# Kernel tuning notes

Measured on AMD Instinct MI355X. Metric: run time of the kernel, lower is better.

The kernel has to match this reference:

```python
import jax, jax.numpy as jnp
import numpy as np

K = 16          # neighbors per query (args.k)
EPS_NORM = 1e-5  # LayerNorm / BatchNorm eps (torch default)


def _knn_edges(xyz, B, n):
    # batch-aware kNN: equal-sized batches, edges never cross batch boundary
    x = xyz.reshape(B, n, 3)
    d2 = jnp.sum((x[:, :, None, :] - x[:, None, :, :]) ** 2, -1)   # [B,n,n]
    _, idx = jax.lax.top_k(-d2, K)                                 # [B,n,K] local neighbor ids
    col = (idx + (jnp.arange(B) * n)[:, None, None]).reshape(-1)   # source (neighbor) [E]
    row = jnp.repeat(jnp.arange(B * n), K)                         # target (query)    [E]
    return row, col


def _forward(support_xyz, batch_index, features, lang_features, mask_flattened,
             W1, b1, ln_g, ln_b, W2, b2,
             Wl1, bl1, bn_g, bn_b, Wl2, bl2,
             Wr1, br1, Wr2, br2, row, col):
    N = support_xyz.shape[0]
    B, L, Fl = lang_features.shape
    # feat_encoder: Linear -> LayerNorm -> ReLU -> Linear
    h = features @ W1 + b1
    mu = h.mean(-1, keepdims=True)
    var = ((h - mu) ** 2).mean(-1, keepdims=True)
    h = (h - mu) / jnp.sqrt(var + EPS_NORM) * ln_g + ln_b
    feats = jax.nn.relu(h) @ W2 + b2                               # [N,F]
    # lang_encoder: Linear -> BatchNorm1d (batch statistics) -> ReLU -> Linear
    hl = lang_features.reshape(B * L, Fl) @ Wl1 + bl1
    mul = hl.mean(0)
    varl = ((hl - mul) ** 2).mean(0)
    hl = (hl - mul) / jnp.sqrt(varl + EPS_NORM) * bn_g + bn_b
    lang = (jax.nn.relu(hl) @ Wl2 + bl2).reshape(B, L, -1)         # [B,L,F]
    lang_flat = lang[batch_index]                                  # [N,L,F]
    # per-point / per-token attention logits
    atten = jnp.einsum('nf,nlf->nl', feats, lang_flat)             # [N,L]
    # segment softmax over incoming kNN edges (CenterOp max / add)
    attenmax = jax.ops.segment_max(atten[col], row, num_segments=N, indices_are_sorted=True)
    a = jnp.exp(atten[col] - attenmax[row])                        # [E,L]
    attensum = jax.ops.segment_sum(a, row, num_segments=N, indices_are_sorted=True)
    # CenterConv message
    att = a / attensum[row] * mask_flattened[row]                  # [E,L]
    att = att / (att.sum(-1, keepdims=True) + 1e-7)
    ctx = jnp.einsum('el,elf->ef', att, lang_flat[col])            # [E,F] attended lang feat
    xi, xj = support_xyz[row], support_xyz[col]
    d = xi - xj
    nrm = jnp.sqrt(jnp.sum(d * d, -1, keepdims=True) + 1e-12)
    ew = jnp.concatenate([xi, xj, d, nrm], -1)                     # [E,10]
    ew = jax.nn.relu(ew @ Wr1 + br1) @ Wr2 + br2                   # [E,F] rel_encoder
    msg = feats[col] * ctx * ew                                    # [E,F]
    rel = jax.ops.segment_sum(msg, row, num_segments=N, indices_are_sorted=True)
    return feats + rel


def setup_inputs() -> dict:
    key = jax.random.key(0)
    ks = jax.random.split(key, 12)
    B, n, L = 4, 1024, 16
    N = B * n
    Fv, Fl, F = 256, 768, 128
    def w(k, shp, fan):
        return jax.random.normal(k, shp, jnp.float32) / np.sqrt(fan).astype(np.float32)
    mask = (jax.random.uniform(ks[3], (N, L)) < 0.8).astype(jnp.float32).at[:, 0].set(1.0)
    return {
        'support_xyz': jax.random.normal(ks[0], (N, 3), jnp.float32),
        'batch_index': jnp.repeat(jnp.arange(B), n),
        'features': jax.random.normal(ks[1], (N, Fv), jnp.float32),
        'lang_features': jax.random.normal(ks[2], (B, L, Fl), jnp.float32),
        'mask_flattened': mask,
        'W1': w(ks[4], (Fv, F), Fv), 'b1': jnp.zeros(F, jnp.float32),
        'ln_g': jnp.ones(F, jnp.float32), 'ln_b': jnp.zeros(F, jnp.float32),
        'W2': w(ks[5], (F, F), F), 'b2': jnp.zeros(F, jnp.float32),
        'Wl1': w(ks[6], (Fl, F), Fl), 'bl1': jnp.zeros(F, jnp.float32),
        'bn_g': jnp.ones(F, jnp.float32), 'bn_b': jnp.zeros(F, jnp.float32),
        'Wl2': w(ks[7], (F, F), F), 'bl2': jnp.zeros(F, jnp.float32),
        'Wr1': w(ks[8], (10, 64), 10), 'br1': jnp.zeros(64, jnp.float32),
        'Wr2': w(ks[9], (64, F), 64), 'br2': jnp.zeros(F, jnp.float32),
    }


def reference(support_xyz, batch_index, features, lang_features, mask_flattened,
              W1, b1, ln_g, ln_b, W2, b2,
              Wl1, bl1, bn_g, bn_b, Wl2, bl2,
              Wr1, br1, Wr2, br2):
    B = lang_features.shape[0]
    n = support_xyz.shape[0] // B
    row, col = _knn_edges(support_xyz, B, n)
    return _forward(support_xyz, batch_index, features, lang_features, mask_flattened,
                    W1, b1, ln_g, ln_b, W2, b2,
                    Wl1, bl1, bn_g, bn_b, Wl2, bl2,
                    Wr1, br1, Wr2, br2, row, col)
```

## Files before the change

### kernel.cpp

```cpp
#include <hip/hip_runtime.h>

typedef unsigned long long u64;
typedef short short8 __attribute__((ext_vector_type(8)));
typedef float f32x4 __attribute__((ext_vector_type(4)));

#define N_PTS   4096
#define B_SZ    4
#define N_PER_B 1024
#define L_TOK   16
#define FV      256
#define FL      768
#define FDIM    128
#define KNN     16
#define RH      64

__device__ __forceinline__ short f2bf(float f) {
    unsigned int x = __float_as_uint(f);
    unsigned int r = (x + 0x7fffu + ((x >> 16) & 1u)) >> 16;
    return (short)r;
}

__global__ __launch_bounds__(256) void k1_kernel(const float* __restrict__ xyz,
                                                 const float* __restrict__ features,
                                                 const float* __restrict__ lf,
                                                 const float* __restrict__ W1,
                                                 const float* __restrict__ b1,
                                                 const float* __restrict__ ln_g,
                                                 const float* __restrict__ ln_b,
                                                 const float* __restrict__ W2,
                                                 const float* __restrict__ b2,
                                                 const float* __restrict__ Wl1,
                                                 const float* __restrict__ bl1,
                                                 int* __restrict__ knn,
                                                 float* __restrict__ feats,
                                                 float* __restrict__ hl) {
    __shared__ float smem[4 * 256 + 4 * 128 + 16];
    int b = blockIdx.x, t = threadIdx.x;

    if (b < 1024) {
        int lane = t & 63;
        int q = b * 4 + (t >> 6);
        int base = (q >> 10) << 10;
        float qx = xyz[q * 3 + 0];
        float qy = xyz[q * 3 + 1];
        float qz = xyz[q * 3 + 2];
        u64 keys[16];
#pragma unroll
        for (int m = 0; m < 16; m++) {
            int j = base + lane + (m << 6);
            float dx = qx - xyz[j * 3 + 0];
            float dy = qy - xyz[j * 3 + 1];
            float dz = qz - xyz[j * 3 + 2];
            float d2 = __fadd_rn(__fadd_rn(__fmul_rn(dx, dx), __fmul_rn(dy, dy)),
                                 __fmul_rn(dz, dz));
            keys[m] = (((u64)__float_as_uint(d2)) << 32) | (unsigned int)j;
        }
        for (int r = 0; r < KNN; r++) {
            u64 lmin = keys[0];
#pragma unroll
            for (int m = 1; m < 16; m++) lmin = (keys[m] < lmin) ? keys[m] : lmin;
            u64 g = lmin;
#pragma unroll
            for (int off = 32; off > 0; off >>= 1) {
                u64 o = __shfl_xor(g, off, 64);
                g = (o < g) ? o : g;
            }
#pragma unroll
            for (int m = 0; m < 16; m++)
                if (keys[m] == g) keys[m] = ~0ULL;
            if (lane == 0) knn[q * KNN + r] = (int)(g & 0xffffffffu);
        }
    } else if (b < 2048) {
        int i0 = (b - 1024) * 4;
        float* fin  = smem;
        float* rbuf = smem + 1024;
        float* red  = smem + 1536;
        for (int p = t; p < 4 * FV; p += 256) {
            int pp = p >> 8, k = p & 255;
            fin[pp * FV + k] = features[(i0 + pp) * FV + k];
        }
        __syncthreads();
        int c = t & 127, h = t >> 7;
        int p0 = 2 * h, p1 = 2 * h + 1;
        float bv = b1[c];
        float acc0 = bv, acc1 = bv;
        for (int k = 0; k < FV; k++) {
            float w = W1[k * FDIM + c];
            acc0 += fin[p0 * FV + k] * w;
            acc1 += fin[p1 * FV + k] * w;
        }
        float s0 = acc0, q0 = acc0 * acc0, s1 = acc1, q1 = acc1 * acc1;
#pragma unroll
        for (int off = 32; off > 0; off >>= 1) {
            s0 += __shfl_xor(s0, off, 64);
            q0 += __shfl_xor(q0, off, 64);
            s1 += __shfl_xor(s1, off, 64);
            q1 += __shfl_xor(q1, off, 64);
        }
        int wid = t >> 6;
        if ((t & 63) == 0) {
            red[wid * 4 + 0] = s0; red[wid * 4 + 1] = q0;
            red[wid * 4 + 2] = s1; red[wid * 4 + 3] = q1;
        }
        __syncthreads();
        float S0 = red[(2 * h) * 4 + 0] + red[(2 * h + 1) * 4 + 0];
        float Q0 = red[(2 * h) * 4 + 1] + red[(2 * h + 1) * 4 + 1];
        float S1 = red[(2 * h) * 4 + 2] + red[(2 * h + 1) * 4 + 2];
        float Q1 = red[(2 * h) * 4 + 3] + red[(2 * h + 1) * 4 + 3];
        float g = ln_g[c], bb = ln_b[c];
        float mu0 = S0 * (1.f / 128.f), var0 = Q0 * (1.f / 128.f) - mu0 * mu0;
        float mu1 = S1 * (1.f / 128.f), var1 = Q1 * (1.f / 128.f) - mu1 * mu1;
        float r0 = fmaxf((acc0 - mu0) * rsqrtf(var0 + 1e-5f) * g + bb, 0.f);
        float r1 = fmaxf((acc1 - mu1) * rsqrtf(var1 + 1e-5f) * g + bb, 0.f);
        rbuf[p0 * FDIM + c] = r0;
        rbuf[p1 * FDIM + c] = r1;
        __syncthreads();
        float b2v = b2[c];
        float f0 = b2v, f1 = b2v;
        for (int k = 0; k < FDIM; k++) {
            float w = W2[k * FDIM + c];
            f0 += rbuf[p0 * FDIM + k] * w;
            f1 += rbuf[p1 * FDIM + k] * w;
        }
        feats[(i0 + p0) * FDIM + c] = f0;
        feats[(i0 + p1) * FDIM + c] = f1;
    } else {
        int r = b - 2048;
        float* lrow = smem;
        float* part = smem + 768;
        for (int k = t; k < FL; k += 256) lrow[k] = lf[r * FL + k];
        __syncthreads();
        int c = t & 127, kh = t >> 7;
        float acc = (kh == 0) ? bl1[c] : 0.f;
        int k0 = kh * 384;
        for (int k = k0; k < k0 + 384; k++) acc += lrow[k] * Wl1[k * FDIM + c];
        part[kh * FDIM + c] = acc;
        __syncthreads();
        if (kh == 0) hl[r * FDIM + c] = part[c] + part[FDIM + c];
    }
}

__global__ __launch_bounds__(128) void lang2_kernel(const float* __restrict__ hl,
                                                    const float* __restrict__ bn_g,
                                                    const float* __restrict__ bn_b,
                                                    const float* __restrict__ Wl2,
                                                    const float* __restrict__ bl2,
                                                    float* __restrict__ lang) {
    __shared__ float rl4[4][FDIM];
    int t = threadIdx.x;
    int r0 = blockIdx.x * 4;
    float s = 0.f, s2 = 0.f;
    for (int r = 0; r < 64; r++) {
        float v = hl[r * FDIM + t];
        s += v; s2 += v * v;
    }
    float mu = s * (1.f / 64.f);
    float var = s2 * (1.f / 64.f) - mu * mu;
    float rs = rsqrtf(var + 1e-5f);
    float g = bn_g[t], bb = bn_b[t];
#pragma unroll
    for (int p = 0; p < 4; p++)
        rl4[p][t] = fmaxf((hl[(r0 + p) * FDIM + t] - mu) * rs * g + bb, 0.f);
    __syncthreads();
    float bv = bl2[t];
    float a0 = bv, a1 = bv, a2 = bv, a3 = bv;
    for (int k = 0; k < FDIM; k++) {
        float w = Wl2[k * FDIM + t];
        a0 += rl4[0][k] * w;
        a1 += rl4[1][k] * w;
        a2 += rl4[2][k] * w;
        a3 += rl4[3][k] * w;
    }
    lang[(r0 + 0) * FDIM + t] = a0;
    lang[(r0 + 1) * FDIM + t] = a1;
    lang[(r0 + 2) * FDIM + t] = a2;
    lang[(r0 + 3) * FDIM + t] = a3;
}

__global__ __launch_bounds__(256) void atten_kernel(const float* __restrict__ feats,
                                                    const float* __restrict__ lang,
                                                    float* __restrict__ atten) {
    __shared__ float fb[2][FDIM];
    __shared__ float pb[256];
    int t = threadIdx.x;
    int half = t >> 7, tt = t & 127;
    int i = blockIdx.x * 2 + half;
    fb[half][tt] = feats[i * FDIM + tt];
    __syncthreads();
    int l = tt >> 3, sj = tt & 7;
    int bi = i >> 10;
    const float* lrow = lang + (bi * L_TOK + l) * FDIM;
    float p = 0.f;
#pragma unroll
    for (int m = 0; m < 16; m++) {
        int k = sj + (m << 3);
        p += fb[half][k] * lrow[k];
    }
    pb[t] = p;
    __syncthreads();
    if (tt < L_TOK) {
        float a = 0.f;
#pragma unroll
        for (int u = 0; u < 8; u++) a += pb[half * 128 + tt * 8 + u];
        atten[i * L_TOK + tt] = a;
    }
}

__global__ __launch_bounds__(256) void edge_kernel(const float* __restrict__ xyz,
                                                   const float* __restrict__ mask,
                                                   const float* __restrict__ Wr1,
                                                   const float* __restrict__ br1,
                                                   const float* __restrict__ Wr2,
                                                   const float* __restrict__ br2,
                                                   const int* __restrict__ knn,
                                                   const float* __restrict__ lang,
                                                   const float* __restrict__ feats,
                                                   const float* __restrict__ atten,
                                                   float* __restrict__ out) {
    int lane = threadIdx.x & 63;
    int wid  = threadIdx.x >> 6;
    int i    = blockIdx.x * 4 + wid;
    int bi   = i >> 10;
    int quad = lane >> 4;
    int e16  = lane & 15;

    int idxe = knn[i * KNN + e16];

    float sat[8];
    if (quad < 2) {
        const float4* ap = (const float4*)(atten + idxe * L_TOK + quad * 8);
        float4 a0 = ap[0], a1 = ap[1];
        sat[0] = a0.x; sat[1] = a0.y; sat[2] = a0.z; sat[3] = a0.w;
        sat[4] = a1.x; sat[5] = a1.y; sat[6] = a1.z; sat[7] = a1.w;
    } else {
#pragma unroll
        for (int j = 0; j < 8; j++) sat[j] = 0.f;
    }

    float mx[8];
#pragma unroll
    for (int j = 0; j < 8; j++) mx[j] = sat[j];
#pragma unroll
    for (int off = 1; off < 16; off <<= 1) {
#pragma unroll
        for (int j = 0; j < 8; j++) mx[j] = fmaxf(mx[j], __shfl_xor(mx[j], off, 16));
    }
    float ex[8], sm[8];
#pragma unroll
    for (int j = 0; j < 8; j++) { ex[j] = __expf(sat[j] - mx[j]); sm[j] = ex[j]; }
#pragma unroll
    for (int off = 1; off < 16; off <<= 1) {
#pragma unroll
        for (int j = 0; j < 8; j++) sm[j] += __shfl_xor(sm[j], off, 16);
    }
    float st[8];
    if (quad < 2) {
        const float4* mp = (const float4*)(mask + i * L_TOK + quad * 8);
        float4 m0 = mp[0], m1 = mp[1];
        float mv[8] = {m0.x, m0.y, m0.z, m0.w, m1.x, m1.y, m1.z, m1.w};
#pragma unroll
        for (int j = 0; j < 8; j++) st[j] = ex[j] * (mv[j] / sm[j]);
    } else {
#pragma unroll
        for (int j = 0; j < 8; j++) st[j] = 0.f;
    }
    float s = st[0] + st[1] + st[2] + st[3] + st[4] + st[5] + st[6] + st[7];
    s += __shfl_xor(s, 16, 64);
    s += __shfl_xor(s, 32, 64);
    float inv2 = 1.f / (s + 1e-7f);
    short8 sattA;
#pragma unroll
    for (int j = 0; j < 8; j++) sattA[j] = f2bf(st[j] * inv2);

    float xi0 = xyz[i * 3 + 0], xi1 = xyz[i * 3 + 1], xi2 = xyz[i * 3 + 2];
    float xj0 = xyz[idxe * 3 + 0], xj1 = xyz[idxe * 3 + 1], xj2 = xyz[idxe * 3 + 2];
    float d0 = xi0 - xj0, d1 = xi1 - xj1, d2v = xi2 - xj2;
    float nr = sqrtf(d0 * d0 + d1 * d1 + d2v * d2v + 1e-12f);
    float ein[10] = {xi0, xi1, xi2, xj0, xj1, xj2, d0, d1, d2v, nr};
    short8 hidA[2];
#pragma unroll
    for (int sstep = 0; sstep < 2; sstep++) {
        int k0 = sstep * 32 + quad * 8;
        float h[8];
        const float4* bp = (const float4*)(br1 + k0);
        float4 b0 = bp[0], b1v = bp[1];
        h[0] = b0.x; h[1] = b0.y; h[2] = b0.z; h[3] = b0.w;
        h[4] = b1v.x; h[5] = b1v.y; h[6] = b1v.z; h[7] = b1v.w;
#pragma unroll
        for (int m = 0; m < 10; m++) {
            const float4* wp = (const float4*)(Wr1 + m * RH + k0);
            float4 w0 = wp[0], w1 = wp[1];
            float em = ein[m];
            h[0] += em * w0.x; h[1] += em * w0.y; h[2] += em * w0.z; h[3] += em * w0.w;
            h[4] += em * w1.x; h[5] += em * w1.y; h[6] += em * w1.z; h[7] += em * w1.w;
        }
#pragma unroll
        for (int j = 0; j < 8; j++) hidA[sstep][j] = f2bf(fmaxf(h[j], 0.f));
    }

    int idxr[4];
#pragma unroll
    for (int r = 0; r < 4; r++) idxr[r] = knn[i * KNN + quad * 4 + r];

#pragma unroll 2
    for (int tile = 0; tile < 8; tile++) {
        int cc = tile * 16 + e16;
        f32x4 accew = {0.f, 0.f, 0.f, 0.f};
#pragma unroll
        for (int sstep = 0; sstep < 2; sstep++) {
            short8 w2B;
#pragma unroll
            for (int j = 0; j < 8; j++)
                w2B[j] = f2bf(Wr2[(sstep * 32 + quad * 8 + j) * FDIM + cc]);
            accew = __builtin_amdgcn_mfma_f32_16x16x32_bf16(hidA[sstep], w2B, accew, 0, 0, 0);
        }
        short8 lsB;
        if (quad < 2) {
#pragma unroll
            for (int j = 0; j < 8; j++)
                lsB[j] = f2bf(lang[bi * L_TOK * FDIM + (quad * 8 + j) * FDIM + cc]);
        } else {
#pragma unroll
            for (int j = 0; j < 8; j++) lsB[j] = 0;
        }
        f32x4 accctx = {0.f, 0.f, 0.f, 0.f};
        accctx = __builtin_amdgcn_mfma_f32_16x16x32_bf16(sattA, lsB, accctx, 0, 0, 0);

        float br2c = br2[cc];
        float msum = 0.f;
#pragma unroll
        for (int r = 0; r < 4; r++) {
            float fj = feats[idxr[r] * FDIM + cc];
            msum += fj * accctx[r] * (accew[r] + br2c);
        }
        msum += __shfl_xor(msum, 16, 64);
        msum += __shfl_xor(msum, 32, 64);
        if (lane < 16)
            out[i * FDIM + cc] = feats[i * FDIM + cc] + msum;
    }
}

extern "C" void kernel_launch(void* const* d_in, const int* in_sizes, int n_in,
                              void* d_out, int out_size, void* d_ws, size_t ws_size,
                              hipStream_t stream) {
    const float* xyz   = (const float*)d_in[0];
    const float* features = (const float*)d_in[2];
    const float* lang_f   = (const float*)d_in[3];
    const float* mask     = (const float*)d_in[4];
    const float* W1   = (const float*)d_in[5];
    const float* b1   = (const float*)d_in[6];
    const float* ln_g = (const float*)d_in[7];
    const float* ln_b = (const float*)d_in[8];
    const float* W2   = (const float*)d_in[9];
    const float* b2   = (const float*)d_in[10];
    const float* Wl1  = (const float*)d_in[11];
    const float* bl1  = (const float*)d_in[12];
    const float* bn_g = (const float*)d_in[13];
    const float* bn_b = (const float*)d_in[14];
    const float* Wl2  = (const float*)d_in[15];
    const float* bl2  = (const float*)d_in[16];
    const float* Wr1  = (const float*)d_in[17];
    const float* br1  = (const float*)d_in[18];
    const float* Wr2  = (const float*)d_in[19];
    const float* br2  = (const float*)d_in[20];

    float* ws_feats = (float*)d_ws;
    float* ws_atten = ws_feats + N_PTS * FDIM;
    float* ws_lang  = ws_atten + N_PTS * L_TOK;
    float* ws_hl    = ws_lang + B_SZ * L_TOK * FDIM;
    int*   ws_knn   = (int*)(ws_hl + 64 * FDIM);

    k1_kernel<<<2112, 256, 0, stream>>>(xyz, features, lang_f,
                                        W1, b1, ln_g, ln_b, W2, b2,
                                        Wl1, bl1, ws_knn, ws_feats, ws_hl);
    lang2_kernel<<<16, 128, 0, stream>>>(ws_hl, bn_g, bn_b, Wl2, bl2, ws_lang);
    atten_kernel<<<N_PTS / 2, 256, 0, stream>>>(ws_feats, ws_lang, ws_atten);
    edge_kernel<<<N_PTS / 4, 256, 0, stream>>>(xyz, mask, Wr1, br1, Wr2, br2,
                                               ws_knn, ws_lang, ws_feats, ws_atten,
                                               (float*)d_out);
}
```

Measured before the change: 165.7 us.

## Fuse feature encoder with attention logits and pre-transpose bf16 weights for edge MFMA

Moves the feature-encoder MLP out of the kNN kernel into a new kernel that processes 16 points per block with float4 register tiling and also computes the per-point attention logits, which removes the separate atten kernel. The first kernel now also writes a transposed bf16 copy of Wr2, and lang2 writes a transposed bf16 copy of lang. This lets the edge kernel load MFMA B operands as single short8 vectors instead of doing strided scalar loads with conversion. It costs an extra kernel dependency stage and some workspace, and the feature MLP no longer overlaps with the kNN blocks.

```diff
diff --git a/kernel.cpp b/kernel.cpp
--- a/kernel.cpp
+++ b/kernel.cpp
@@ -19,22 +19,19 @@
     unsigned int r = (x + 0x7fffu + ((x >> 16) & 1u)) >> 16;
     return (short)r;
 }
-
-__global__ __launch_bounds__(256) void k1_kernel(const float* __restrict__ xyz,
-                                                 const float* __restrict__ features,
+__device__ __forceinline__ void fma4(float4& a, float s, const float4 w) {
+    a.x += s * w.x; a.y += s * w.y; a.z += s * w.z; a.w += s * w.w;
+}
+
+__global__ __launch_bounds__(256) void kA_kernel(const float* __restrict__ xyz,
                                                  const float* __restrict__ lf,
-                                                 const float* __restrict__ W1,
-                                                 const float* __restrict__ b1,
-                                                 const float* __restrict__ ln_g,
-                                                 const float* __restrict__ ln_b,
-                                                 const float* __restrict__ W2,
-                                                 const float* __restrict__ b2,
                                                  const float* __restrict__ Wl1,
                                                  const float* __restrict__ bl1,
+                                                 const float* __restrict__ Wr2,
                                                  int* __restrict__ knn,
-                                                 float* __restrict__ feats,
-                                                 float* __restrict__ hl) {
-    __shared__ float smem[4 * 256 + 4 * 128 + 16];
+                                                 float* __restrict__ hl,
+                                                 short* __restrict__ wr2t) {
+    __shared__ float smem[1024];
     int b = blockIdx.x, t = threadIdx.x;
 
     if (b < 1024) {
@@ -70,62 +67,8 @@
                 if (keys[m] == g) keys[m] = ~0ULL;
             if (lane == 0) knn[q * KNN + r] = (int)(g & 0xffffffffu);
         }
-    } else if (b < 2048) {
-        int i0 = (b - 1024) * 4;
-        float* fin  = smem;
-        float* rbuf = smem + 1024;
-        float* red  = smem + 1536;
-        for (int p = t; p < 4 * FV; p += 256) {
-            int pp = p >> 8, k = p & 255;
-            fin[pp * FV + k] = features[(i0 + pp) * FV + k];
-        }
-        __syncthreads();
-        int c = t & 127, h = t >> 7;
-        int p0 = 2 * h, p1 = 2 * h + 1;
-        float bv = b1[c];
-        float acc0 = bv, acc1 = bv;
-        for (int k = 0; k < FV; k++) {
-            float w = W1[k * FDIM + c];
-            acc0 += fin[p0 * FV + k] * w;
-            acc1 += fin[p1 * FV + k] * w;
-        }
-        float s0 = acc0, q0 = acc0 * acc0, s1 = acc1, q1 = acc1 * acc1;
-#pragma unroll
-        for (int off = 32; off > 0; off >>= 1) {
-            s0 += __shfl_xor(s0, off, 64);
-            q0 += __shfl_xor(q0, off, 64);
-            s1 += __shfl_xor(s1, off, 64);
-            q1 += __shfl_xor(q1, off, 64);
-        }
-        int wid = t >> 6;
-        if ((t & 63) == 0) {
-            red[wid * 4 + 0] = s0; red[wid * 4 + 1] = q0;
-            red[wid * 4 + 2] = s1; red[wid * 4 + 3] = q1;
-        }
-        __syncthreads();
-        float S0 = red[(2 * h) * 4 + 0] + red[(2 * h + 1) * 4 + 0];
-        float Q0 = red[(2 * h) * 4 + 1] + red[(2 * h + 1) * 4 + 1];
-        float S1 = red[(2 * h) * 4 + 2] + red[(2 * h + 1) * 4 + 2];
-        float Q1 = red[(2 * h) * 4 + 3] + red[(2 * h + 1) * 4 + 3];
-        float g = ln_g[c], bb = ln_b[c];
-        float mu0 = S0 * (1.f / 128.f), var0 = Q0 * (1.f / 128.f) - mu0 * mu0;
-        float mu1 = S1 * (1.f / 128.f), var1 = Q1 * (1.f / 128.f) - mu1 * mu1;
-        float r0 = fmaxf((acc0 - mu0) * rsqrtf(var0 + 1e-5f) * g + bb, 0.f);
-        float r1 = fmaxf((acc1 - mu1) * rsqrtf(var1 + 1e-5f) * g + bb, 0.f);
-        rbuf[p0 * FDIM + c] = r0;
-        rbuf[p1 * FDIM + c] = r1;
-        __syncthreads();
-        float b2v = b2[c];
-        float f0 = b2v, f1 = b2v;
-        for (int k = 0; k < FDIM; k++) {
-            float w = W2[k * FDIM + c];
-            f0 += rbuf[p0 * FDIM + k] * w;
-            f1 += rbuf[p1 * FDIM + k] * w;
-        }
-        feats[(i0 + p0) * FDIM + c] = f0;
-        feats[(i0 + p1) * FDIM + c] = f1;
-    } else {
-        int r = b - 2048;
+    } else if (b < 1088) {
+        int r = b - 1024;
         float* lrow = smem;
         float* part = smem + 768;
         for (int k = t; k < FL; k += 256) lrow[k] = lf[r * FL + k];
@@ -137,6 +80,11 @@
         part[kh * FDIM + c] = acc;
         __syncthreads();
         if (kh == 0) hl[r * FDIM + c] = part[c] + part[FDIM + c];
+    } else {
+        for (int p = t; p < RH * FDIM; p += 256) {
+            int c = p >> 6, k = p & 63;
+            wr2t[c * RH + k] = f2bf(Wr2[k * FDIM + c]);
+        }
     }
 }
 
@@ -145,7 +93,8 @@
                                                     const float* __restrict__ bn_b,
                                                     const float* __restrict__ Wl2,
                                                     const float* __restrict__ bl2,
-                                                    float* __restrict__ lang) {
+                                                    float* __restrict__ lang,
+                                                    short* __restrict__ langT) {
     __shared__ float rl4[4][FDIM];
     int t = threadIdx.x;
     int r0 = blockIdx.x * 4;
@@ -163,57 +112,128 @@
         rl4[p][t] = fmaxf((hl[(r0 + p) * FDIM + t] - mu) * rs * g + bb, 0.f);
     __syncthreads();
     float bv = bl2[t];
-    float a0 = bv, a1 = bv, a2 = bv, a3 = bv;
+    float a[4] = {bv, bv, bv, bv};
     for (int k = 0; k < FDIM; k++) {
         float w = Wl2[k * FDIM + t];
-        a0 += rl4[0][k] * w;
-        a1 += rl4[1][k] * w;
-        a2 += rl4[2][k] * w;
-        a3 += rl4[3][k] * w;
-    }
-    lang[(r0 + 0) * FDIM + t] = a0;
-    lang[(r0 + 1) * FDIM + t] = a1;
-    lang[(r0 + 2) * FDIM + t] = a2;
-    lang[(r0 + 3) * FDIM + t] = a3;
-}
-
-__global__ __launch_bounds__(256) void atten_kernel(const float* __restrict__ feats,
-                                                    const float* __restrict__ lang,
-                                                    float* __restrict__ atten) {
-    __shared__ float fb[2][FDIM];
-    __shared__ float pb[256];
+        a[0] += rl4[0][k] * w;
+        a[1] += rl4[1][k] * w;
+        a[2] += rl4[2][k] * w;
+        a[3] += rl4[3][k] * w;
+    }
+#pragma unroll
+    for (int p = 0; p < 4; p++) {
+        int r = r0 + p;
+        lang[r * FDIM + t] = a[p];
+        langT[((r >> 4) * FDIM + t) * L_TOK + (r & 15)] = f2bf(a[p]);
+    }
+}
+
+__global__ __launch_bounds__(256) void feat_kernel(const float* __restrict__ features,
+                                                   const float* __restrict__ W1,
+                                                   const float* __restrict__ b1,
+                                                   const float* __restrict__ ln_g,
+                                                   const float* __restrict__ ln_b,
+                                                   const float* __restrict__ W2,
+                                                   const float* __restrict__ b2,
+                                                   const float* __restrict__ lang,
+                                                   float* __restrict__ feats,
+                                                   float* __restrict__ atten) {
+    __shared__ float fin[16 * FV];
+    __shared__ float rbuf[16 * FDIM];
+    __shared__ float fbuf[16 * FDIM];
     int t = threadIdx.x;
-    int half = t >> 7, tt = t & 127;
-    int i = blockIdx.x * 2 + half;
-    fb[half][tt] = feats[i * FDIM + tt];
+    int i0 = blockIdx.x * 16;
+    {
+        const float4* src = (const float4*)(features + i0 * FV);
+        float4* dst = (float4*)fin;
+#pragma unroll
+        for (int v = 0; v < 4; v++) dst[t + 256 * v] = src[t + 256 * v];
+    }
     __syncthreads();
-    int l = tt >> 3, sj = tt & 7;
-    int bi = i >> 10;
-    const float* lrow = lang + (bi * L_TOK + l) * FDIM;
-    float p = 0.f;
-#pragma unroll
-    for (int m = 0; m < 16; m++) {
-        int k = sj + (m << 3);
-        p += fb[half][k] * lrow[k];
-    }
-    pb[t] = p;
+    int cg = t & 31, ps = t >> 5;
+    int c0 = cg * 4;
+    int p0 = ps * 2, p1 = p0 + 1;
+
+    float4 bv = *(const float4*)(b1 + c0);
+    float4 a0 = bv, a1 = bv;
+    for (int k4 = 0; k4 < FV / 4; k4++) {
+        float4 f0 = *(const float4*)&fin[p0 * FV + k4 * 4];
+        float4 f1 = *(const float4*)&fin[p1 * FV + k4 * 4];
+        const float* wp = W1 + (k4 * 4) * FDIM + c0;
+        float4 w;
+        w = *(const float4*)(wp);            fma4(a0, f0.x, w); fma4(a1, f1.x, w);
+        w = *(const float4*)(wp + FDIM);     fma4(a0, f0.y, w); fma4(a1, f1.y, w);
+        w = *(const float4*)(wp + 2 * FDIM); fma4(a0, f0.z, w); fma4(a1, f1.z, w);
+        w = *(const float4*)(wp + 3 * FDIM); fma4(a0, f0.w, w); fma4(a1, f1.w, w);
+    }
+    float s0 = a0.x + a0.y + a0.z + a0.w;
+    float q0 = a0.x * a0.x + a0.y * a0.y + a0.z * a0.z + a0.w * a0.w;
+    float s1 = a1.x + a1.y + a1.z + a1.w;
+    float q1 = a1.x * a1.x + a1.y * a1.y + a1.z * a1.z + a1.w * a1.w;
+#pragma unroll
+    for (int off = 1; off < 32; off <<= 1) {
+        s0 += __shfl_xor(s0, off, 32);
+        q0 += __shfl_xor(q0, off, 32);
+        s1 += __shfl_xor(s1, off, 32);
+        q1 += __shfl_xor(q1, off, 32);
+    }
+    float mu0 = s0 * (1.f / 128.f), var0 = q0 * (1.f / 128.f) - mu0 * mu0;
+    float mu1 = s1 * (1.f / 128.f), var1 = q1 * (1.f / 128.f) - mu1 * mu1;
+    float rs0 = rsqrtf(var0 + 1e-5f), rs1 = rsqrtf(var1 + 1e-5f);
+    float4 g4 = *(const float4*)(ln_g + c0);
+    float4 lb4 = *(const float4*)(ln_b + c0);
+    float4 r0v, r1v;
+    r0v.x = fmaxf((a0.x - mu0) * rs0 * g4.x + lb4.x, 0.f);
+    r0v.y = fmaxf((a0.y - mu0) * rs0 * g4.y + lb4.y, 0.f);
+    r0v.z = fmaxf((a0.z - mu0) * rs0 * g4.z + lb4.z, 0.f);
+    r0v.w = fmaxf((a0.w - mu0) * rs0 * g4.w + lb4.w, 0.f);
+    r1v.x = fmaxf((a1.x - mu1) * rs1 * g4.x + lb4.x, 0.f);
+    r1v.y = fmaxf((a1.y - mu1) * rs1 * g4.y + lb4.y, 0.f);
+    r1v.z = fmaxf((a1.z - mu1) * rs1 * g4.z + lb4.z, 0.f);
+    r1v.w = fmaxf((a1.w - mu1) * rs1 * g4.w + lb4.w, 0.f);
+    *(float4*)&rbuf[p0 * FDIM + c0] = r0v;
+    *(float4*)&rbuf[p1 * FDIM + c0] = r1v;
     __syncthreads();
-    if (tt < L_TOK) {
-        float a = 0.f;
-#pragma unroll
-        for (int u = 0; u < 8; u++) a += pb[half * 128 + tt * 8 + u];
-        atten[i * L_TOK + tt] = a;
-    }
+
+    float4 bv2 = *(const float4*)(b2 + c0);
+    float4 o0 = bv2, o1 = bv2;
+    for (int k4 = 0; k4 < FDIM / 4; k4++) {
+        float4 f0 = *(const float4*)&rbuf[p0 * FDIM + k4 * 4];
+        float4 f1 = *(const float4*)&rbuf[p1 * FDIM + k4 * 4];
+        const float* wp = W2 + (k4 * 4) * FDIM + c0;
+        float4 w;
+        w = *(const float4*)(wp);            fma4(o0, f0.x, w); fma4(o1, f1.x, w);
+        w = *(const float4*)(wp + FDIM);     fma4(o0, f0.y, w); fma4(o1, f1.y, w);
+        w = *(const float4*)(wp + 2 * FDIM); fma4(o0, f0.z, w); fma4(o1, f1.z, w);
+        w = *(const float4*)(wp + 3 * FDIM); fma4(o0, f0.w, w); fma4(o1, f1.w, w);
+    }
+    *(float4*)(feats + (i0 + p0) * FDIM + c0) = o0;
+    *(float4*)(feats + (i0 + p1) * FDIM + c0) = o1;
+    *(float4*)&fbuf[p0 * FDIM + c0] = o0;
+    *(float4*)&fbuf[p1 * FDIM + c0] = o1;
+    __syncthreads();
+
+    int p = t >> 4, l = t & 15;
+    int bi = i0 >> 10;
+    const float4* lr = (const float4*)(lang + (bi * L_TOK + l) * FDIM);
+    const float4* fr = (const float4*)&fbuf[p * FDIM];
+    float acc = 0.f;
+#pragma unroll
+    for (int k = 0; k < FDIM / 4; k++) {
+        float4 x = lr[k], y = fr[k];
+        acc += x.x * y.x + x.y * y.y + x.z * y.z + x.w * y.w;
+    }
+    atten[(i0 + p) * L_TOK + l] = acc;
 }
 
 __global__ __launch_bounds__(256) void edge_kernel(const float* __restrict__ xyz,
                                                    const float* __restrict__ mask,
                                                    const float* __restrict__ Wr1,
                                                    const float* __restrict__ br1,
-                                                   const float* __restrict__ Wr2,
+                                                   const short* __restrict__ wr2t,
                                                    const float* __restrict__ br2,
                                                    const int* __restrict__ knn,
-                                                   const float* __restrict__ lang,
+                                                   const short* __restrict__ langT,
                                                    const float* __restrict__ feats,
                                                    const float* __restrict__ atten,
                                                    float* __restrict__ out) {
@@ -305,20 +325,13 @@
 #pragma unroll 2
     for (int tile = 0; tile < 8; tile++) {
         int cc = tile * 16 + e16;
+        const short8* w2p = (const short8*)(wr2t + cc * RH);
         f32x4 accew = {0.f, 0.f, 0.f, 0.f};
-#pragma unroll
-        for (int sstep = 0; sstep < 2; sstep++) {
-            short8 w2B;
-#pragma unroll
-            for (int j = 0; j < 8; j++)
-                w2B[j] = f2bf(Wr2[(sstep * 32 + quad * 8 + j) * FDIM + cc]);
-            accew = __builtin_amdgcn_mfma_f32_16x16x32_bf16(hidA[sstep], w2B, accew, 0, 0, 0);
-        }
+        accew = __builtin_amdgcn_mfma_f32_16x16x32_bf16(hidA[0], w2p[quad],     accew, 0, 0, 0);
+        accew = __builtin_amdgcn_mfma_f32_16x16x32_bf16(hidA[1], w2p[4 + quad], accew, 0, 0, 0);
         short8 lsB;
         if (quad < 2) {
-#pragma unroll
-            for (int j = 0; j < 8; j++)
-                lsB[j] = f2bf(lang[bi * L_TOK * FDIM + (quad * 8 + j) * FDIM + cc]);
+            lsB = ((const short8*)(langT + (bi * FDIM + cc) * L_TOK))[quad];
         } else {
 #pragma unroll
             for (int j = 0; j < 8; j++) lsB[j] = 0;
@@ -369,13 +382,16 @@
     float* ws_lang  = ws_atten + N_PTS * L_TOK;
     float* ws_hl    = ws_lang + B_SZ * L_TOK * FDIM;
     int*   ws_knn   = (int*)(ws_hl + 64 * FDIM);
-
-    k1_kernel<<<2112, 256, 0, stream>>>(xyz, features, lang_f,
-                                        W1, b1, ln_g, ln_b, W2, b2,
-                                        Wl1, bl1, ws_knn, ws_feats, ws_hl);
-    lang2_kernel<<<16, 128, 0, stream>>>(ws_hl, bn_g, bn_b, Wl2, bl2, ws_lang);
-    atten_kernel<<<N_PTS / 2, 256, 0, stream>>>(ws_feats, ws_lang, ws_atten);
-    edge_kernel<<<N_PTS / 4, 256, 0, stream>>>(xyz, mask, Wr1, br1, Wr2, br2,
-                                               ws_knn, ws_lang, ws_feats, ws_atten,
+    short* ws_wr2t  = (short*)(ws_knn + N_PTS * KNN);
+    short* ws_langT = ws_wr2t + FDIM * RH;
+
+    kA_kernel<<<1089, 256, 0, stream>>>(xyz, lang_f, Wl1, bl1, Wr2,
+                                        ws_knn, ws_hl, ws_wr2t);
+    lang2_kernel<<<16, 128, 0, stream>>>(ws_hl, bn_g, bn_b, Wl2, bl2,
+                                         ws_lang, ws_langT);
+    feat_kernel<<<N_PTS / 16, 256, 0, stream>>>(features, W1, b1, ln_g, ln_b, W2, b2,
+                                                ws_lang, ws_feats, ws_atten);
+    edge_kernel<<<N_PTS / 4, 256, 0, stream>>>(xyz, mask, Wr1, br1, ws_wr2t, br2,
+                                               ws_knn, ws_langT, ws_feats, ws_atten,
                                                (float*)d_out);
 }
```

Result: slower. 174.2 us (+5.1%).
